# Optimization experiments

Hardware: AMD Instinct MI355X
Metric: run time of the kernel (lower is better)

## Reference

```python
import jax, jax.numpy as jnp
import numpy as np

HEADS, DIM, N = 16, 128, 2048
NEG = -1e9


def setup_inputs() -> dict:
    key = jax.random.key(0)
    ks = jax.random.split(key, 8)
    xavier = lambda k, shape, fan: jax.random.uniform(
        k, shape, jnp.float32, -1.0, 1.0) * np.sqrt(6.0 / fan)
    return {
        "q": jax.random.normal(ks[0], (N, DIM), jnp.float32),
        "k": jax.random.normal(ks[1], (N, DIM), jnp.float32),
        "v": jax.random.normal(ks[2], (N, DIM), jnp.float32),
        "mask": jax.random.randint(ks[3], (N, N), 0, 2) > 0,
        "Q": xavier(ks[4], (HEADS, DIM, DIM), 2 * DIM),
        "K": xavier(ks[5], (HEADS, DIM, DIM), 2 * DIM),
        "V": xavier(ks[6], (HEADS, DIM, DIM), 2 * DIM),
        "last": xavier(ks[7], (HEADS * DIM, DIM), HEADS * DIM + DIM),
    }


def reference(q, k, v, Q, K, V, last, mask):
    # per-head projections: [n, d] x [h, d, d] -> [h, n, d]
    qp = jnp.einsum('nd,hde->hne', q, Q)
    kp = jnp.einsum('nd,hde->hne', k, K)
    vp = jnp.einsum('nd,hde->hne', v, V)
    n = qp.shape[1]
    # NOTE: original computes k @ q^T and scales by sqrt(seq_len) (q.size(1) after projection)
    att = jnp.einsum('hid,hjd->hij', kp, qp)  # [h, n, n]
    fmask = mask.astype(jnp.float32)
    att = att * fmask / jnp.sqrt(jnp.float32(n)) + NEG * (1.0 - fmask)
    att = jax.nn.softmax(att, axis=2)
    out = jnp.einsum('hij,hjd->hid', att, vp)            # [h, n, d]
    out = jnp.transpose(out, (1, 0, 2)).reshape(n, -1)   # n (heads d)
    return out @ last
```

## Files before the change

### kernel.cpp

```cpp
#include <hip/hip_runtime.h>
#include <hip/hip_bf16.h>


#define HN 16
#define NN 2048
#define DD 128

typedef __attribute__((ext_vector_type(8))) short short8;
typedef __attribute__((ext_vector_type(4))) short short4v;
typedef __attribute__((ext_vector_type(4))) float float4v;
typedef __attribute__((ext_vector_type(16))) float f32x16;
typedef __attribute__((ext_vector_type(4))) unsigned int uint4v;

#define CROW(r) ((((r) & 3)) + 8 * ((r) >> 2))

__device__ inline unsigned short f2bf(float f) {
    unsigned int u = __builtin_bit_cast(unsigned int, f);
    unsigned int r = (u + 0x7fffu + ((u >> 16) & 1u)) >> 16;
    return (unsigned short)r;
}

__device__ inline unsigned int cvtpk(float lo, float hi) {
    unsigned int w;
    asm("v_cvt_pk_bf16_f32 %0, %1, %2" : "=v"(w) : "v"(lo), "v"(hi));
    return w;
}

__device__ inline void plswap(unsigned int& x, unsigned int& y) {
#if __has_builtin(__builtin_amdgcn_permlane32_swap)
    typedef int int2v __attribute__((ext_vector_type(2)));
    int2v r = __builtin_amdgcn_permlane32_swap((int)x, (int)y, false, false);
    x = (unsigned int)r[0];
    y = (unsigned int)r[1];
#else
    const unsigned int sx = (unsigned int)__shfl_xor((int)x, 32);
    const unsigned int sy = (unsigned int)__shfl_xor((int)y, 32);
    const bool hiHalf = (threadIdx.x & 32) != 0;
    const unsigned int nx = hiHalf ? sy : x;
    const unsigned int ny = hiHalf ? y : sx;
    x = nx; y = ny;
#endif
}

__device__ inline short8 ld_bf8(const float* __restrict__ p) {
    const float4v a = *(const float4v*)p;
    const float4v b = *(const float4v*)(p + 4);
    short8 r;
    r[0] = (short)f2bf(a[0]); r[1] = (short)f2bf(a[1]);
    r[2] = (short)f2bf(a[2]); r[3] = (short)f2bf(a[3]);
    r[4] = (short)f2bf(b[0]); r[5] = (short)f2bf(b[1]);
    r[6] = (short)f2bf(b[2]); r[7] = (short)f2bf(b[3]);
    return r;
}

__device__ inline short8 ld2x4(const unsigned short* p) {
    const short4v lo = *(const short4v*)p;
    const short4v hi = *(const short4v*)(p + 4);
    short8 r;
    r[0] = lo[0]; r[1] = lo[1]; r[2] = lo[2]; r[3] = lo[3];
    r[4] = hi[0]; r[5] = hi[1]; r[6] = hi[2]; r[7] = hi[3];
    return r;
}

__global__ void sentinel_kernel(float* out, int n) {
    int i = blockIdx.x * 256 + threadIdx.x;
    if (i < n) out[i] = 2.0f;
}

__global__ __launch_bounds__(256) void maskpack2_kernel(
    const int* __restrict__ mask,
    unsigned long long* __restrict__ mbT,
    float* __restrict__ out, int out_n)
{
    const int wgrp = blockIdx.x * 4 + (threadIdx.x >> 6);
    const int lane = threadIdx.x & 63;
    const int word0 = wgrp * 4;
    const int i = word0 >> 5;
    const int w = word0 & 31;
    const int* row = mask + (size_t)i * NN + w * 64;
    unsigned long long b[4];
#pragma unroll
    for (int c = 0; c < 4; c++)
        b[c] = __ballot(row[c * 64 + lane] != 0);
    if (lane == 0) {
#pragma unroll
        for (int c = 0; c < 4; c++) mbT[(size_t)(w + c) * NN + i] = b[c];
    }
    const int z = blockIdx.x * 256 + threadIdx.x;
    if (z < out_n) out[z] = 0.f;
}

__global__ __launch_bounds__(256) void wprep_kernel(
    const float* __restrict__ Qw,
    const float* __restrict__ Kw,
    const float* __restrict__ Vw,
    unsigned short* __restrict__ wsW)
{
    __shared__ __align__(16) unsigned short Wt[128 * 132];
    const int h = blockIdx.x, t = blockIdx.y;
    const float* W = ((t == 0) ? Qw : ((t == 1) ? Kw : Vw)) + h * DD * DD;
    unsigned short* o = wsW + ((size_t)t * HN + h) * DD * DD;
    const int tid = threadIdx.x;

    for (int idx2 = tid * 2; idx2 < DD * DD; idx2 += 512) {
        const int d = idx2 >> 7, e = idx2 & 127;
        const float2 w2 = *(const float2*)(W + idx2);
        Wt[(e + 0) * 132 + d] = f2bf(w2.x);
        Wt[(e + 1) * 132 + d] = f2bf(w2.y);
    }
    __syncthreads();
    for (int idx8 = tid * 8; idx8 < DD * DD; idx8 += 2048) {
        const int e = idx8 >> 7, d = idx8 & 127;
        *(short8*)(o + idx8) = ld2x4(&Wt[e * 132 + d]);
    }
}

__global__ __launch_bounds__(256) void proj4_kernel(
    const float* __restrict__ q,
    const float* __restrict__ k,
    const float* __restrict__ v,
    const unsigned short* __restrict__ wsW,
    unsigned short* __restrict__ ws)
{
    __shared__ __align__(16) unsigned short Wt[128 * 136];
    const int t = blockIdx.z, h = blockIdx.y, cb = blockIdx.x;
    const int tid = threadIdx.x;
    const float* in = (t == 0) ? q : ((t == 1) ? k : v);
    const unsigned short* WTg = wsW + ((size_t)t * HN + h) * DD * DD;
    unsigned short* out = ws + (size_t)t * (HN * NN * DD) + (size_t)h * (NN * DD);

#pragma unroll
    for (int it = 0; it < 8; it++) {
        const int idx8 = tid * 8 + it * 2048;
        const int row = idx8 >> 7, col = idx8 & 127;
        *(short8*)(&Wt[row * 136 + col]) = *(const short8*)(WTg + idx8);
    }
    __syncthreads();

    const int wave = tid >> 6, lane = tid & 63;
    const int quad = lane >> 4, l16 = lane & 15;

#pragma unroll 1
    for (int rt = 0; rt < 2; rt++) {
        const int row0 = cb * 128 + rt * 64 + wave * 16;

        float4v acc[8];
#pragma unroll
        for (int c = 0; c < 8; c++) acc[c] = {0.f, 0.f, 0.f, 0.f};

        if (t < 2) {
#pragma unroll
            for (int kk = 0; kk < 4; kk++) {
                const short8 a = ld_bf8(in + (size_t)(row0 + l16) * DD + kk * 32 + quad * 8);
#pragma unroll
                for (int c = 0; c < 8; c++) {
                    const short8 b = *(const short8*)(&Wt[(c * 16 + l16) * 136 + kk * 32 + quad * 8]);
                    acc[c] = __builtin_amdgcn_mfma_f32_16x16x32_bf16(a, b, acc[c], 0, 0, 0);
                }
            }
            if (t == 0) {
#pragma unroll
                for (int c = 0; c < 8; c++)
#pragma unroll
                    for (int r = 0; r < 4; r++) {
                        const int row = row0 + quad * 4 + r;
                        out[(size_t)(((row >> 5) * 8 + c)) * 512 + (row & 31) * 16 + l16]
                            = f2bf(acc[c][r]);
                    }
            } else {
#pragma unroll
                for (int c = 0; c < 8; c++)
#pragma unroll
                    for (int r = 0; r < 4; r++)
                        out[(size_t)(row0 + quad * 4 + r) * DD + c * 16 + l16] = f2bf(acc[c][r]);
            }
        } else {
#pragma unroll
            for (int kk = 0; kk < 4; kk++) {
                const short8 bv = ld_bf8(in + (size_t)(row0 + l16) * DD + kk * 32 + quad * 8);
#pragma unroll
                for (int c = 0; c < 8; c++) {
                    const short8 aw = *(const short8*)(&Wt[(c * 16 + l16) * 136 + kk * 32 + quad * 8]);
                    acc[c] = __builtin_amdgcn_mfma_f32_16x16x32_bf16(aw, bv, acc[c], 0, 0, 0);
                }
            }
#pragma unroll
            for (int c = 0; c < 8; c++)
#pragma unroll
                for (int r = 0; r < 4; r++) {
                    const int d = c * 16 + quad * 4 + r;
                    out[(size_t)(row0 >> 4) * 2048 + d * 16 + l16] = f2bf(acc[c][r]);
                }
        }
    }
}

__global__ __launch_bounds__(256, 2) void attn_kernel(
    unsigned short* __restrict__ ws,
    const unsigned long long* __restrict__ mbT)
{
    __shared__ __align__(16) float obuf[8192];
    __shared__ float lbuf[192];

    const int h = blockIdx.y, ib = blockIdx.x;
    const int tid = threadIdx.x;
    const int wave = tid >> 6, lane = tid & 63;
    const int ig = wave >> 1;
    const int h2 = wave & 1;
    const int l31 = lane & 31;
    const int hi = lane >> 5;

    const unsigned short* qA  = ws + (size_t)h * (NN * DD);
    const unsigned short* kp  = ws + (size_t)(HN * NN * DD) + (size_t)h * (NN * DD);
    const unsigned short* vpB = ws + (size_t)(2 * HN * NN * DD) + (size_t)h * (NN * DD);
    unsigned short* ao = ws + (size_t)(3 * HN * NN * DD);

    const int i0 = ib * 64;
    const float scale = 0.022097086912079612f;

    short8 kpf[8];
    {
        const int row = i0 + ig * 32 + l31;
#pragma unroll
        for (int kk = 0; kk < 8; kk++)
            kpf[kk] = *(const short8*)(kp + (size_t)row * DD + kk * 16 + hi * 8);
    }

    const unsigned short* qbase = qA + l31 * 16 + hi * 8;
    const unsigned short* vbase = vpB + l31 * 16 + hi * 8;

    f32x16 o[4];
#pragma unroll
    for (int dt = 0; dt < 4; dt++)
#pragma unroll
        for (int r = 0; r < 16; r++) o[dt][r] = 0.f;
    float lacc = 0.f;

    short8 qfA[8], qfB[8];

#define QLD(QF, JT) do {                                                        \
        const unsigned short* p_ = qbase + (size_t)(((JT) * 2 + h2) * 8) * 512; \
        _Pragma("unroll")                                                       \
        for (int kk = 0; kk < 8; kk++)                                          \
            QF[kk] = *(const short8*)(p_ + kk * 512);                           \
    } while (0)

    auto COMPUTE = [&](const short8 (&qf)[8], int jt) {
        short8 vf[8];
#pragma unroll
        for (int ks = 0; ks < 2; ks++)
#pragma unroll
            for (int dt = 0; dt < 4; dt++)
                vf[ks * 4 + dt] = *(const short8*)(vbase
                    + (size_t)(jt * 4 + h2 * 2 + ks) * 2048 + dt * 512);
        const unsigned long long mrow = mbT[(size_t)jt * NN + i0 + ig * 32 + l31];
        const unsigned int m2 = (unsigned int)(mrow >> (h2 * 32 + hi * 4));

        f32x16 s;
#pragma unroll
        for (int r = 0; r < 16; r++) s[r] = 0.f;
        __builtin_amdgcn_s_setprio(1);
#pragma unroll
        for (int kk = 0; kk < 8; kk++)
            s = __builtin_amdgcn_mfma_f32_32x32x16_bf16(qf[kk], kpf[kk], s, 0, 0, 0);
        __builtin_amdgcn_s_setprio(0);

#pragma unroll
        for (int r = 0; r < 16; r++) {
            const float x = ((m2 >> CROW(r)) & 1u) ? fmaf(s[r], scale, -5.0f) : -50.0f;
            s[r] = __expf(x);
        }
        float ls = (((s[0] + s[1]) + (s[2] + s[3])) + ((s[4] + s[5]) + (s[6] + s[7])))
                 + (((s[8] + s[9]) + (s[10] + s[11])) + ((s[12] + s[13]) + (s[14] + s[15])));
        ls += __shfl_xor(ls, 32);
        lacc += ls;

        short8 pa[2];
#pragma unroll
        for (int ks = 0; ks < 2; ks++) {
            const int b = ks * 8;
            unsigned int x0 = cvtpk(s[b + 0], s[b + 1]);
            unsigned int y0 = cvtpk(s[b + 4], s[b + 5]);
            unsigned int x1 = cvtpk(s[b + 2], s[b + 3]);
            unsigned int y1 = cvtpk(s[b + 6], s[b + 7]);
            plswap(x0, y0);
            plswap(x1, y1);
            uint4v w; w[0] = x0; w[1] = x1; w[2] = y0; w[3] = y1;
            pa[ks] = __builtin_bit_cast(short8, w);
        }

        __builtin_amdgcn_s_setprio(1);
#pragma unroll
        for (int ks = 0; ks < 2; ks++)
#pragma unroll
            for (int dt = 0; dt < 4; dt++)
                o[dt] = __builtin_amdgcn_mfma_f32_32x32x16_bf16(pa[ks], vf[ks * 4 + dt], o[dt], 0, 0, 0);
        __builtin_amdgcn_s_setprio(0);
    };

    QLD(qfA, 0);
#pragma unroll 1
    for (int jt = 0; jt < 32; jt += 2) {
        QLD(qfB, jt + 1);
        COMPUTE(qfA, jt);
        if (jt + 2 < 32) QLD(qfA, jt + 2);
        COMPUTE(qfB, jt + 1);
    }
#undef QLD

    if (h2 == 1) {
#pragma unroll
        for (int dt = 0; dt < 4; dt++)
#pragma unroll
            for (int r = 0; r < 16; r++)
                obuf[(((ig * 2 + hi) * 4 + dt) * 16 + r) * 32 + l31] = o[dt][r];
        if (hi == 0) lbuf[ig * 32 + l31] = lacc;
    }
    __syncthreads();
    if (h2 == 0) {
        const float lt = lacc + lbuf[ig * 32 + l31];
        const float inv = (lt > 0.f) ? (1.0f / lt) : 0.f;
        if (hi == 0) lbuf[64 + ig * 32 + l31] = inv;
#pragma unroll
        for (int dt = 0; dt < 4; dt++)
#pragma unroll
            for (int r = 0; r < 16; r++) {
                const int row = CROW(r) + hi * 4;
                const float val = (o[dt][r] + obuf[(((ig * 2 + hi) * 4 + dt) * 16 + r) * 32 + l31])
                                  * lbuf[64 + ig * 32 + row];
                ao[(size_t)(i0 + ig * 32 + row) * (HN * DD) + h * DD + dt * 32 + l31] = f2bf(val);
            }
    }
}

__global__ __launch_bounds__(256) void final2_kernel(
    const unsigned short* __restrict__ ao,
    const float* __restrict__ last,
    float* __restrict__ outp)
{
    __shared__ __align__(16) unsigned short lt[32 * 516];
    const int tid = threadIdx.x;
    const int wave = tid >> 6, lane = tid & 63;
    const int quad = lane >> 4, l16 = lane & 15;
    const int i0 = blockIdx.x * 64;
    const int e0 = blockIdx.y * 32;
    const int k0 = blockIdx.z * 512;

#pragma unroll
    for (int idx2 = tid * 2; idx2 < 512 * 32; idx2 += 512) {
        const int kk = idx2 >> 5, e = idx2 & 31;
        const float2 w2 = *(const float2*)(last + (size_t)(k0 + kk) * DD + e0 + e);
        lt[(e + 0) * 516 + kk] = f2bf(w2.x);
        lt[(e + 1) * 516 + kk] = f2bf(w2.y);
    }
    __syncthreads();

    float4v acc[2];
    acc[0] = {0.f, 0.f, 0.f, 0.f};
    acc[1] = {0.f, 0.f, 0.f, 0.f};

    const unsigned short* arow = ao + (size_t)(i0 + wave * 16 + l16) * (HN * DD) + k0;

#pragma unroll
    for (int kb = 0; kb < 8; kb++) {
#pragma unroll
        for (int ks = 0; ks < 2; ks++) {
            const short8 a = *(const short8*)(arow + kb * 64 + ks * 32 + quad * 8);
#pragma unroll
            for (int dc = 0; dc < 2; dc++) {
                const short8 b = ld2x4(&lt[(dc * 16 + l16) * 516 + kb * 64 + ks * 32 + quad * 8]);
                acc[dc] = __builtin_amdgcn_mfma_f32_16x16x32_bf16(a, b, acc[dc], 0, 0, 0);
            }
        }
    }

#pragma unroll
    for (int r = 0; r < 4; r++)
#pragma unroll
        for (int dc = 0; dc < 2; dc++)
            atomicAdd(&outp[(size_t)(i0 + wave * 16 + quad * 4 + r) * DD + e0 + dc * 16 + l16],
                      acc[dc][r]);
}

extern "C" void kernel_launch(void* const* d_in, const int* in_sizes, int n_in,
                              void* d_out, int out_size, void* d_ws, size_t ws_size,
                              hipStream_t stream)
{
    const float* q    = (const float*)d_in[0];
    const float* k    = (const float*)d_in[1];
    const float* v    = (const float*)d_in[2];
    const int*   mask = (const int*)d_in[3];
    const float* Qw   = (const float*)d_in[4];
    const float* Kw   = (const float*)d_in[5];
    const float* Vw   = (const float*)d_in[6];
    const float* last = (const float*)d_in[7];
    unsigned short* ws  = (unsigned short*)d_ws;
    float* out = (float*)d_out;

    const size_t shorts_main = (size_t)4 * HN * NN * DD;
    const size_t mb_bytes = (size_t)NN * (NN / 64) * 8;
    const size_t needed = shorts_main * sizeof(unsigned short) + mb_bytes;
    if (ws_size < needed) {
        sentinel_kernel<<<(out_size + 255) / 256, 256, 0, stream>>>(out, out_size);
        return;
    }
    unsigned long long* mbT = (unsigned long long*)(ws + shorts_main);
    unsigned short* wsW = ws + (size_t)3 * HN * NN * DD;

    maskpack2_kernel<<<dim3(NN * (NN / 64) / 16), 256, 0, stream>>>(mask, mbT, out, out_size);
    wprep_kernel<<<dim3(16, 3), 256, 0, stream>>>(Qw, Kw, Vw, wsW);
    proj4_kernel<<<dim3(16, 16, 3), 256, 0, stream>>>(q, k, v, wsW, ws);
    attn_kernel<<<dim3(32, 16), 256, 0, stream>>>(ws, mbT);
    final2_kernel<<<dim3(32, 4, 4), 256, 0, stream>>>(ws + (size_t)3 * HN * NN * DD, last, out);
}
```

Before: 160.5 us.

## Split attention key range across four waves per row group with tree reduction

The attention kernel moves from 256 to 512 threads per block, so each 32-row query group now has four waves instead of two, each covering a quarter of the key slices. The partial outputs and row sums are combined through shared memory in a two-step tree reduction with extra barriers. The softmax exponent also switches to exp2f with the scale, bias and masked value pre-multiplied by log2(e). This raises wave-level parallelism for the 512-block grid, at the cost of more shared memory, more reduction traffic and tighter register limits from launch_bounds(512,4).

```diff
diff --git a/kernel.cpp b/kernel.cpp
--- a/kernel.cpp
+++ b/kernel.cpp
@@ -195,18 +195,19 @@
     }
 }
 
-__global__ __launch_bounds__(256, 2) void attn_kernel(
+__global__ __launch_bounds__(512, 4) void attn_kernel(
     unsigned short* __restrict__ ws,
     const unsigned long long* __restrict__ mbT)
 {
-    __shared__ __align__(16) float obuf[8192];
-    __shared__ float lbuf[192];
+    __shared__ __align__(16) float obufA[2][4096];
+    __shared__ __align__(16) float obufB[2][4096];
+    __shared__ float lbuf[2 * 96 + 64];
 
     const int h = blockIdx.y, ib = blockIdx.x;
     const int tid = threadIdx.x;
     const int wave = tid >> 6, lane = tid & 63;
-    const int ig = wave >> 1;
-    const int h2 = wave & 1;
+    const int ig = wave >> 2;
+    const int jq = wave & 3;
     const int l31 = lane & 31;
     const int hi = lane >> 5;
 
@@ -216,7 +217,9 @@
     unsigned short* ao = ws + (size_t)(3 * HN * NN * DD);
 
     const int i0 = ib * 64;
-    const float scale = 0.022097086912079612f;
+    const float scale2 = 0.031879347175f;
+    const float bias2  = -7.2134752044f;
+    const float neg2   = -72.134752044f;
 
     short8 kpf[8];
     {
@@ -238,23 +241,23 @@
 
     short8 qfA[8], qfB[8];
 
-#define QLD(QF, JT) do {                                                        \
-        const unsigned short* p_ = qbase + (size_t)(((JT) * 2 + h2) * 8) * 512; \
+#define QLD(QF, SLICE) do {                                                     \
+        const unsigned short* p_ = qbase + (size_t)((SLICE) * 8) * 512;         \
         _Pragma("unroll")                                                       \
         for (int kk = 0; kk < 8; kk++)                                          \
             QF[kk] = *(const short8*)(p_ + kk * 512);                           \
     } while (0)
 
-    auto COMPUTE = [&](const short8 (&qf)[8], int jt) {
+    auto COMPUTE = [&](const short8 (&qf)[8], int slice) {
         short8 vf[8];
 #pragma unroll
         for (int ks = 0; ks < 2; ks++)
 #pragma unroll
             for (int dt = 0; dt < 4; dt++)
                 vf[ks * 4 + dt] = *(const short8*)(vbase
-                    + (size_t)(jt * 4 + h2 * 2 + ks) * 2048 + dt * 512);
-        const unsigned long long mrow = mbT[(size_t)jt * NN + i0 + ig * 32 + l31];
-        const unsigned int m2 = (unsigned int)(mrow >> (h2 * 32 + hi * 4));
+                    + (size_t)(slice * 2 + ks) * 2048 + dt * 512);
+        const unsigned long long mrow = mbT[(size_t)(slice >> 1) * NN + i0 + ig * 32 + l31];
+        const unsigned int m2 = (unsigned int)(mrow >> ((slice & 1) * 32 + hi * 4));
 
         f32x16 s;
 #pragma unroll
@@ -267,8 +270,8 @@
 
 #pragma unroll
         for (int r = 0; r < 16; r++) {
-            const float x = ((m2 >> CROW(r)) & 1u) ? fmaf(s[r], scale, -5.0f) : -50.0f;
-            s[r] = __expf(x);
+            const float x = ((m2 >> CROW(r)) & 1u) ? fmaf(s[r], scale2, bias2) : neg2;
+            s[r] = exp2f(x);
         }
         float ls = (((s[0] + s[1]) + (s[2] + s[3])) + ((s[4] + s[5]) + (s[6] + s[7])))
                  + (((s[8] + s[9]) + (s[10] + s[11])) + ((s[12] + s[13]) + (s[14] + s[15])));
@@ -298,39 +301,66 @@
         __builtin_amdgcn_s_setprio(0);
     };
 
-    QLD(qfA, 0);
+    QLD(qfA, jq);
 #pragma unroll 1
-    for (int jt = 0; jt < 32; jt += 2) {
-        QLD(qfB, jt + 1);
-        COMPUTE(qfA, jt);
-        if (jt + 2 < 32) QLD(qfA, jt + 2);
-        COMPUTE(qfB, jt + 1);
+    for (int it = 0; it < 16; it += 2) {
+        QLD(qfB, (it + 1) * 4 + jq);
+        COMPUTE(qfA, it * 4 + jq);
+        if (it + 2 < 16) QLD(qfA, (it + 2) * 4 + jq);
+        COMPUTE(qfB, (it + 1) * 4 + jq);
     }
 #undef QLD
 
-    if (h2 == 1) {
+#define OIDX(dt, r) ((((hi) * 4 + (dt)) * 16 + (r)) * 32 + l31)
+    if (jq == 1 || jq == 3) {
+        float* dst = (jq == 1) ? &obufA[ig][0] : &obufB[ig][0];
 #pragma unroll
         for (int dt = 0; dt < 4; dt++)
 #pragma unroll
             for (int r = 0; r < 16; r++)
-                obuf[(((ig * 2 + hi) * 4 + dt) * 16 + r) * 32 + l31] = o[dt][r];
-        if (hi == 0) lbuf[ig * 32 + l31] = lacc;
-    }
-    __syncthreads();
-    if (h2 == 0) {
-        const float lt = lacc + lbuf[ig * 32 + l31];
+                dst[OIDX(dt, r)] = o[dt][r];
+    }
+    if (jq != 0 && hi == 0) lbuf[ig * 96 + (jq - 1) * 32 + l31] = lacc;
+    __syncthreads();
+    if (jq == 0) {
+#pragma unroll
+        for (int dt = 0; dt < 4; dt++)
+#pragma unroll
+            for (int r = 0; r < 16; r++)
+                o[dt][r] += obufA[ig][OIDX(dt, r)];
+    }
+    if (jq == 2) {
+#pragma unroll
+        for (int dt = 0; dt < 4; dt++)
+#pragma unroll
+            for (int r = 0; r < 16; r++)
+                o[dt][r] += obufB[ig][OIDX(dt, r)];
+    }
+    __syncthreads();
+    if (jq == 2) {
+#pragma unroll
+        for (int dt = 0; dt < 4; dt++)
+#pragma unroll
+            for (int r = 0; r < 16; r++)
+                obufA[ig][OIDX(dt, r)] = o[dt][r];
+    }
+    __syncthreads();
+    if (jq == 0) {
+        const float lt = lacc + lbuf[ig * 96 + l31] + lbuf[ig * 96 + 32 + l31]
+                       + lbuf[ig * 96 + 64 + l31];
         const float inv = (lt > 0.f) ? (1.0f / lt) : 0.f;
-        if (hi == 0) lbuf[64 + ig * 32 + l31] = inv;
+        float* linv = &lbuf[192];
+        if (hi == 0) linv[ig * 32 + l31] = inv;
 #pragma unroll
         for (int dt = 0; dt < 4; dt++)
 #pragma unroll
             for (int r = 0; r < 16; r++) {
                 const int row = CROW(r) + hi * 4;
-                const float val = (o[dt][r] + obuf[(((ig * 2 + hi) * 4 + dt) * 16 + r) * 32 + l31])
-                                  * lbuf[64 + ig * 32 + row];
+                const float val = (o[dt][r] + obufA[ig][OIDX(dt, r)]) * linv[ig * 32 + row];
                 ao[(size_t)(i0 + ig * 32 + row) * (HN * DD) + h * DD + dt * 32 + l31] = f2bf(val);
             }
     }
+#undef OIDX
 }
 
 __global__ __launch_bounds__(256) void final2_kernel(
@@ -410,6 +440,6 @@
     maskpack2_kernel<<<dim3(NN * (NN / 64) / 16), 256, 0, stream>>>(mask, mbT, out, out_size);
     wprep_kernel<<<dim3(16, 3), 256, 0, stream>>>(Qw, Kw, Vw, wsW);
     proj4_kernel<<<dim3(16, 16, 3), 256, 0, stream>>>(q, k, v, wsW, ws);
-    attn_kernel<<<dim3(32, 16), 256, 0, stream>>>(ws, mbT);
+    attn_kernel<<<dim3(32, 16), 512, 0, stream>>>(ws, mbT);
     final2_kernel<<<dim3(32, 4, 4), 256, 0, stream>>>(ws + (size_t)3 * HN * NN * DD, last, out);
 }
```

Result: slower. 402.3 us (+150.6%).

## Split attention output dim across two blocks, raise occupancy, use exp2

Applied to the files above, without the earlier changes.

Adds a third grid dimension so each attention block computes only half of the 128-wide output columns. This halves the accumulator registers and LDS use and lets launch bounds target 4 blocks per CU. The cost is that QK^T scores and softmax are now computed twice, once per half. The Q double-buffer prefetch is removed, and exp is rewritten as exp2 with prescaled constants.

```diff
diff --git a/kernel.cpp b/kernel.cpp
--- a/kernel.cpp
+++ b/kernel.cpp
@@ -195,14 +195,14 @@
     }
 }
 
-__global__ __launch_bounds__(256, 2) void attn_kernel(
+__global__ __launch_bounds__(256, 4) void attn_kernel(
     unsigned short* __restrict__ ws,
     const unsigned long long* __restrict__ mbT)
 {
-    __shared__ __align__(16) float obuf[8192];
+    __shared__ __align__(16) float obuf[2][2048];
     __shared__ float lbuf[192];
 
-    const int h = blockIdx.y, ib = blockIdx.x;
+    const int h = blockIdx.y, ib = blockIdx.x, dh = blockIdx.z;
     const int tid = threadIdx.x;
     const int wave = tid >> 6, lane = tid & 63;
     const int ig = wave >> 1;
@@ -216,7 +216,9 @@
     unsigned short* ao = ws + (size_t)(3 * HN * NN * DD);
 
     const int i0 = ib * 64;
-    const float scale = 0.022097086912079612f;
+    const float scale2 = 0.031879347175f;
+    const float bias2  = -7.2134752044f;
+    const float neg2   = -72.134752044f;
 
     short8 kpf[8];
     {
@@ -229,30 +231,30 @@
     const unsigned short* qbase = qA + l31 * 16 + hi * 8;
     const unsigned short* vbase = vpB + l31 * 16 + hi * 8;
 
-    f32x16 o[4];
-#pragma unroll
-    for (int dt = 0; dt < 4; dt++)
+    f32x16 o[2];
+#pragma unroll
+    for (int dt = 0; dt < 2; dt++)
 #pragma unroll
         for (int r = 0; r < 16; r++) o[dt][r] = 0.f;
     float lacc = 0.f;
 
-    short8 qfA[8], qfB[8];
-
-#define QLD(QF, JT) do {                                                        \
-        const unsigned short* p_ = qbase + (size_t)(((JT) * 2 + h2) * 8) * 512; \
-        _Pragma("unroll")                                                       \
-        for (int kk = 0; kk < 8; kk++)                                          \
-            QF[kk] = *(const short8*)(p_ + kk * 512);                           \
-    } while (0)
-
-    auto COMPUTE = [&](const short8 (&qf)[8], int jt) {
-        short8 vf[8];
+    short8 qf[8];
+
+#pragma unroll 1
+    for (int jt = 0; jt < 32; ++jt) {
+        {
+            const unsigned short* p_ = qbase + (size_t)((jt * 2 + h2) * 8) * 512;
+#pragma unroll
+            for (int kk = 0; kk < 8; kk++)
+                qf[kk] = *(const short8*)(p_ + kk * 512);
+        }
+        short8 vf[4];
 #pragma unroll
         for (int ks = 0; ks < 2; ks++)
 #pragma unroll
-            for (int dt = 0; dt < 4; dt++)
-                vf[ks * 4 + dt] = *(const short8*)(vbase
-                    + (size_t)(jt * 4 + h2 * 2 + ks) * 2048 + dt * 512);
+            for (int dt = 0; dt < 2; dt++)
+                vf[ks * 2 + dt] = *(const short8*)(vbase
+                    + (size_t)(jt * 4 + h2 * 2 + ks) * 2048 + (dh * 2 + dt) * 512);
         const unsigned long long mrow = mbT[(size_t)jt * NN + i0 + ig * 32 + l31];
         const unsigned int m2 = (unsigned int)(mrow >> (h2 * 32 + hi * 4));
 
@@ -267,8 +269,8 @@
 
 #pragma unroll
         for (int r = 0; r < 16; r++) {
-            const float x = ((m2 >> CROW(r)) & 1u) ? fmaf(s[r], scale, -5.0f) : -50.0f;
-            s[r] = __expf(x);
+            const float x = ((m2 >> CROW(r)) & 1u) ? fmaf(s[r], scale2, bias2) : neg2;
+            s[r] = exp2f(x);
         }
         float ls = (((s[0] + s[1]) + (s[2] + s[3])) + ((s[4] + s[5]) + (s[6] + s[7])))
                  + (((s[8] + s[9]) + (s[10] + s[11])) + ((s[12] + s[13]) + (s[14] + s[15])));
@@ -293,27 +295,18 @@
 #pragma unroll
         for (int ks = 0; ks < 2; ks++)
 #pragma unroll
-            for (int dt = 0; dt < 4; dt++)
-                o[dt] = __builtin_amdgcn_mfma_f32_32x32x16_bf16(pa[ks], vf[ks * 4 + dt], o[dt], 0, 0, 0);
+            for (int dt = 0; dt < 2; dt++)
+                o[dt] = __builtin_amdgcn_mfma_f32_32x32x16_bf16(pa[ks], vf[ks * 2 + dt], o[dt], 0, 0, 0);
         __builtin_amdgcn_s_setprio(0);
-    };
-
-    QLD(qfA, 0);
-#pragma unroll 1
-    for (int jt = 0; jt < 32; jt += 2) {
-        QLD(qfB, jt + 1);
-        COMPUTE(qfA, jt);
-        if (jt + 2 < 32) QLD(qfA, jt + 2);
-        COMPUTE(qfB, jt + 1);
-    }
-#undef QLD
-
+    }
+
+#define OIDX(dt, r) ((((hi) * 2 + (dt)) * 16 + (r)) * 32 + l31)
     if (h2 == 1) {
 #pragma unroll
-        for (int dt = 0; dt < 4; dt++)
+        for (int dt = 0; dt < 2; dt++)
 #pragma unroll
             for (int r = 0; r < 16; r++)
-                obuf[(((ig * 2 + hi) * 4 + dt) * 16 + r) * 32 + l31] = o[dt][r];
+                obuf[ig][OIDX(dt, r)] = o[dt][r];
         if (hi == 0) lbuf[ig * 32 + l31] = lacc;
     }
     __syncthreads();
@@ -322,15 +315,16 @@
         const float inv = (lt > 0.f) ? (1.0f / lt) : 0.f;
         if (hi == 0) lbuf[64 + ig * 32 + l31] = inv;
 #pragma unroll
-        for (int dt = 0; dt < 4; dt++)
+        for (int dt = 0; dt < 2; dt++)
 #pragma unroll
             for (int r = 0; r < 16; r++) {
                 const int row = CROW(r) + hi * 4;
-                const float val = (o[dt][r] + obuf[(((ig * 2 + hi) * 4 + dt) * 16 + r) * 32 + l31])
-                                  * lbuf[64 + ig * 32 + row];
-                ao[(size_t)(i0 + ig * 32 + row) * (HN * DD) + h * DD + dt * 32 + l31] = f2bf(val);
+                const float val = (o[dt][r] + obuf[ig][OIDX(dt, r)]) * lbuf[64 + ig * 32 + row];
+                ao[(size_t)(i0 + ig * 32 + row) * (HN * DD) + h * DD + dh * 64 + dt * 32 + l31]
+                    = f2bf(val);
             }
     }
+#undef OIDX
 }
 
 __global__ __launch_bounds__(256) void final2_kernel(
@@ -410,6 +404,6 @@
     maskpack2_kernel<<<dim3(NN * (NN / 64) / 16), 256, 0, stream>>>(mask, mbT, out, out_size);
     wprep_kernel<<<dim3(16, 3), 256, 0, stream>>>(Qw, Kw, Vw, wsW);
     proj4_kernel<<<dim3(16, 16, 3), 256, 0, stream>>>(q, k, v, wsW, ws);
-    attn_kernel<<<dim3(32, 16), 256, 0, stream>>>(ws, mbT);
+    attn_kernel<<<dim3(32, 16, 2), 256, 0, stream>>>(ws, mbT);
     final2_kernel<<<dim3(32, 4, 4), 256, 0, stream>>>(ws + (size_t)3 * HN * NN * DD, last, out);
 }
```

Measured after the change: 242.0 us. 1.51x slower.

## Software-pipeline QK MFMA one tile ahead of softmax/PV and use exp2

Applied to the files above, without the earlier changes.

Restructures the attention inner loop so the QK^T MFMA for the next key tile is issued before the softmax and PV MFMAs of the current tile, with the mask load also prefetched one step ahead. The goal is to overlap the exp/convert ALU work with matrix-core work and hide load latency. Softmax constants are also folded into the log2 domain so exp2f is used instead of __expf. This holds an extra score accumulator live, which raises register pressure and may reduce occupancy.

```diff
diff --git a/kernel.cpp b/kernel.cpp
--- a/kernel.cpp
+++ b/kernel.cpp
@@ -216,7 +216,9 @@
     unsigned short* ao = ws + (size_t)(3 * HN * NN * DD);
 
     const int i0 = ib * 64;
-    const float scale = 0.022097086912079612f;
+    const float scale2 = 0.031879347175f;
+    const float bias2  = -7.2134752044f;
+    const float neg2   = -72.134752044f;
 
     short8 kpf[8];
     {
@@ -228,6 +230,7 @@
 
     const unsigned short* qbase = qA + l31 * 16 + hi * 8;
     const unsigned short* vbase = vpB + l31 * 16 + hi * 8;
+    const unsigned long long* mbase = mbT + i0 + ig * 32 + l31;
 
     f32x16 o[4];
 #pragma unroll
@@ -236,26 +239,18 @@
         for (int r = 0; r < 16; r++) o[dt][r] = 0.f;
     float lacc = 0.f;
 
-    short8 qfA[8], qfB[8];
-
-#define QLD(QF, JT) do {                                                        \
-        const unsigned short* p_ = qbase + (size_t)(((JT) * 2 + h2) * 8) * 512; \
+    short8 q0[8], q1[8];
+    f32x16 s0, s1;
+    unsigned long long m0, m1;
+
+#define QLD(QF, T) do {                                                         \
+        const unsigned short* p_ = qbase + (size_t)((((T) * 2 + h2)) * 8) * 512;\
         _Pragma("unroll")                                                       \
         for (int kk = 0; kk < 8; kk++)                                          \
             QF[kk] = *(const short8*)(p_ + kk * 512);                           \
     } while (0)
 
-    auto COMPUTE = [&](const short8 (&qf)[8], int jt) {
-        short8 vf[8];
-#pragma unroll
-        for (int ks = 0; ks < 2; ks++)
-#pragma unroll
-            for (int dt = 0; dt < 4; dt++)
-                vf[ks * 4 + dt] = *(const short8*)(vbase
-                    + (size_t)(jt * 4 + h2 * 2 + ks) * 2048 + dt * 512);
-        const unsigned long long mrow = mbT[(size_t)jt * NN + i0 + ig * 32 + l31];
-        const unsigned int m2 = (unsigned int)(mrow >> (h2 * 32 + hi * 4));
-
+    auto QKC = [&](const short8 (&qf)[8]) -> f32x16 {
         f32x16 s;
 #pragma unroll
         for (int r = 0; r < 16; r++) s[r] = 0.f;
@@ -264,14 +259,27 @@
         for (int kk = 0; kk < 8; kk++)
             s = __builtin_amdgcn_mfma_f32_32x32x16_bf16(qf[kk], kpf[kk], s, 0, 0, 0);
         __builtin_amdgcn_s_setprio(0);
-
+        return s;
+    };
+
+    auto SMPV = [&](const f32x16& sv, unsigned long long mrow, int t) {
+        short8 vf[8];
+#pragma unroll
+        for (int ks = 0; ks < 2; ks++)
+#pragma unroll
+            for (int dt = 0; dt < 4; dt++)
+                vf[ks * 4 + dt] = *(const short8*)(vbase
+                    + (size_t)(t * 4 + h2 * 2 + ks) * 2048 + dt * 512);
+        const unsigned int m2 = (unsigned int)(mrow >> (h2 * 32 + hi * 4));
+
+        f32x16 p;
 #pragma unroll
         for (int r = 0; r < 16; r++) {
-            const float x = ((m2 >> CROW(r)) & 1u) ? fmaf(s[r], scale, -5.0f) : -50.0f;
-            s[r] = __expf(x);
+            const float x = ((m2 >> CROW(r)) & 1u) ? fmaf(sv[r], scale2, bias2) : neg2;
+            p[r] = exp2f(x);
         }
-        float ls = (((s[0] + s[1]) + (s[2] + s[3])) + ((s[4] + s[5]) + (s[6] + s[7])))
-                 + (((s[8] + s[9]) + (s[10] + s[11])) + ((s[12] + s[13]) + (s[14] + s[15])));
+        float ls = (((p[0] + p[1]) + (p[2] + p[3])) + ((p[4] + p[5]) + (p[6] + p[7])))
+                 + (((p[8] + p[9]) + (p[10] + p[11])) + ((p[12] + p[13]) + (p[14] + p[15])));
         ls += __shfl_xor(ls, 32);
         lacc += ls;
 
@@ -279,10 +287,10 @@
 #pragma unroll
         for (int ks = 0; ks < 2; ks++) {
             const int b = ks * 8;
-            unsigned int x0 = cvtpk(s[b + 0], s[b + 1]);
-            unsigned int y0 = cvtpk(s[b + 4], s[b + 5]);
-            unsigned int x1 = cvtpk(s[b + 2], s[b + 3]);
-            unsigned int y1 = cvtpk(s[b + 6], s[b + 7]);
+            unsigned int x0 = cvtpk(p[b + 0], p[b + 1]);
+            unsigned int y0 = cvtpk(p[b + 4], p[b + 5]);
+            unsigned int x1 = cvtpk(p[b + 2], p[b + 3]);
+            unsigned int y1 = cvtpk(p[b + 6], p[b + 7]);
             plswap(x0, y0);
             plswap(x1, y1);
             uint4v w; w[0] = x0; w[1] = x1; w[2] = y0; w[3] = y1;
@@ -298,14 +306,27 @@
         __builtin_amdgcn_s_setprio(0);
     };
 
-    QLD(qfA, 0);
+    QLD(q0, 0);
+    QLD(q1, 1);
+    m0 = mbase[0];
+    s0 = QKC(q0);
+
 #pragma unroll 1
-    for (int jt = 0; jt < 32; jt += 2) {
-        QLD(qfB, jt + 1);
-        COMPUTE(qfA, jt);
-        if (jt + 2 < 32) QLD(qfA, jt + 2);
-        COMPUTE(qfB, jt + 1);
-    }
+    for (int t = 0; t < 30; t += 2) {
+        QLD(q0, t + 2);
+        m1 = mbase[(size_t)(t + 1) * NN];
+        s1 = QKC(q1);
+        SMPV(s0, m0, t);
+        QLD(q1, t + 3);
+        m0 = mbase[(size_t)(t + 2) * NN];
+        s0 = QKC(q0);
+        SMPV(s1, m1, t + 1);
+    }
+    m1 = mbase[(size_t)31 * NN];
+    s1 = QKC(q1);
+    SMPV(s0, m0, 30);
+    SMPV(s1, m1, 31);
+
 #undef QLD
 
     if (h2 == 1) {
```

After: 165.4 us. 1.03x slower.
